# Optimization experiments

Measured on AMD Instinct MI355X. Metric: run time of the kernel, lower is better.

## Reference

```python
import jax, jax.numpy as jnp
import numpy as np

B, N, J, D, H = 64, 128, 512, 1024, 4096
ITERS, EPS = 3, 1e-8
SCALE = D ** -0.5
LN_EPS = 1e-5  # torch LayerNorm default


def _ln(x, g, b):
    m = jnp.mean(x, axis=-1, keepdims=True)
    v = jnp.mean((x - m) ** 2, axis=-1, keepdims=True)
    return (x - m) * jax.lax.rsqrt(v + LN_EPS) * g + b


def setup_inputs() -> dict:
    key = jax.random.key(0)
    ks = jax.random.split(key, 24)
    p = lambda i, shape: jax.random.normal(ks[i], shape, jnp.float32) * 0.02
    return {
        "inputs": jax.random.normal(ks[0], (B, N, D), jnp.float32),
        "texts": jax.random.normal(ks[1], (J, D), jnp.float32),
        "Wq": p(2, (D, D)), "bq": jnp.zeros((D,), jnp.float32),
        "Wk": p(3, (D, D)), "bk": jnp.zeros((D,), jnp.float32),
        "Wv": p(4, (D, D)), "bv": jnp.zeros((D,), jnp.float32),
        "W_ih": p(5, (3 * D, D)), "b_ih": jnp.zeros((3 * D,), jnp.float32),
        "W_hh": p(6, (3 * D, D)), "b_hh": jnp.zeros((3 * D,), jnp.float32),
        "W1": p(7, (H, D)), "b1": jnp.zeros((H,), jnp.float32),
        "W2": p(8, (D, H)), "b2": jnp.zeros((D,), jnp.float32),
        "g_in": jnp.ones((D,), jnp.float32), "be_in": jnp.zeros((D,), jnp.float32),
        "g_sl": jnp.ones((D,), jnp.float32), "be_sl": jnp.zeros((D,), jnp.float32),
        "g_ff": jnp.ones((D,), jnp.float32), "be_ff": jnp.zeros((D,), jnp.float32),
    }


def reference(inputs, texts, Wq, bq, Wk, bk, Wv, bv, W_ih, b_ih, W_hh, b_hh,
              W1, b1, W2, b2, g_in, be_in, g_sl, be_sl, g_ff, be_ff):
    slots = inputs                                  # [B, N, D]
    texts_n = _ln(texts, g_in, be_in)               # [J, D] (repeat == broadcast)
    k = texts_n @ Wk.T + bk                         # [J, D]
    v = texts_n @ Wv.T + bv                         # [J, D]
    for _ in range(ITERS):
        slots_prev = slots
        q = _ln(slots, g_sl, be_sl) @ Wq.T + bq     # [B, N, D]
        dots = jnp.einsum('bid,jd->bij', q, k) * SCALE
        attn = jax.nn.softmax(dots, axis=1) + EPS   # softmax over slots dim
        attn = attn / jnp.sum(attn, axis=-1, keepdims=True)
        updates = jnp.einsum('jd,bij->bid', v, attn)
        # GRUCell: input=updates, hidden=slots_prev (torch gate order r, z, n)
        gi = updates @ W_ih.T + b_ih
        gh = slots_prev @ W_hh.T + b_hh
        i_r, i_z, i_n = jnp.split(gi, 3, axis=-1)
        h_r, h_z, h_n = jnp.split(gh, 3, axis=-1)
        r = jax.nn.sigmoid(i_r + h_r)
        z = jax.nn.sigmoid(i_z + h_z)
        n = jnp.tanh(i_n + r * h_n)
        slots = (1.0 - z) * n + z * slots_prev
        ff = _ln(slots, g_ff, be_ff)
        slots = slots + (jax.nn.relu(ff @ W1.T + b1) @ W2.T + b2)
    return slots
```

## Files before the change

### kernel.cpp

```cpp
#include <hip/hip_runtime.h>
#include <hip/hip_bf16.h>
#include <stdint.h>


using bf16 = __hip_bfloat16;
typedef __bf16 bf16x8 __attribute__((ext_vector_type(8)));
typedef float f32x4 __attribute__((ext_vector_type(4)));

#define F_RELU    1
#define F_SIGMOID 2
#define F_GRU     4
#define F_EPSC    8

__device__ __forceinline__ void gl_to_lds16(const void* g, void* l) {
  __builtin_amdgcn_global_load_lds(
      (const __attribute__((address_space(1))) uint32_t*)(uintptr_t)g,
      (__attribute__((address_space(3))) uint32_t*)(uintptr_t)l,
      16, 0, 0);
}

template <int BN>
__global__ __launch_bounds__(256, 4) void gemm_bt(
    const bf16* __restrict__ X, int ldx,
    const bf16* __restrict__ W, int ldw,
    const float* __restrict__ bias,
    int M, int N, int K, float scale, int flags,
    float* __restrict__ outF, int ldf,
    bf16* __restrict__ outB, int ldb,
    const float* __restrict__ resid,
    const bf16* __restrict__ rz,
    const bf16* __restrict__ hn,
    const float* __restrict__ auxA,
    const float* __restrict__ auxB)
{
  constexpr int NJ = BN / 32;
  __shared__ __align__(16) bf16 As[128 * 64];
  __shared__ __align__(16) bf16 Bs[BN * 64];
  const int t = threadIdx.x;
  const int m0 = blockIdx.x * 128, n0 = blockIdx.y * BN;
  const int wave = t >> 6, lane = t & 63;
  const int wm = (wave >> 1) * 64, wn = (wave & 1) * (BN / 2);
  const int lrow = lane & 15, quad = lane >> 4;

  f32x4 acc[4][NJ] = {};

  const int srow = t >> 3;
  const int scol = ((t & 7) ^ (srow & 7)) * 8;
  const bf16* Ag = X + (size_t)(m0 + srow) * ldx + scol;
  const bf16* Bg = W + (size_t)(n0 + srow) * ldw + scol;
  bf16* Al = As + t * 8;
  bf16* Bl = Bs + t * 8;

  const int r3 = lrow & 7;
  const int c0 = quad ^ r3;
  const int c1 = (4 + quad) ^ r3;

  for (int k0 = 0; k0 < K; k0 += 64) {
#pragma unroll
    for (int u = 0; u < 4; ++u)
      gl_to_lds16(Ag + k0 + (size_t)(u * 32) * ldx, Al + u * 2048);
#pragma unroll
    for (int u = 0; u < NJ; ++u)
      gl_to_lds16(Bg + k0 + (size_t)(u * 32) * ldw, Bl + u * 2048);
    __syncthreads();
    const bf16x8* AS = (const bf16x8*)As;
    const bf16x8* BS = (const bf16x8*)Bs;
#pragma unroll
    for (int kk = 0; kk < 2; ++kk) {
      const int ck = kk ? c1 : c0;
      bf16x8 af[4], bfr[NJ];
#pragma unroll
      for (int i = 0; i < 4; i++)  af[i]  = AS[(wm + i * 16 + lrow) * 8 + ck];
#pragma unroll
      for (int j = 0; j < NJ; j++) bfr[j] = BS[(wn + j * 16 + lrow) * 8 + ck];
#pragma unroll
      for (int i = 0; i < 4; i++)
#pragma unroll
        for (int j = 0; j < NJ; j++)
          acc[i][j] = __builtin_amdgcn_mfma_f32_16x16x32_bf16(af[i], bfr[j], acc[i][j], 0, 0, 0);
    }
    __syncthreads();
  }

#pragma unroll
  for (int i = 0; i < 4; i++) {
    const int row0 = m0 + wm + i * 16 + quad * 4;
#pragma unroll
    for (int j = 0; j < NJ; j++) {
      const int col = n0 + wn + j * 16 + lrow;
      const float badd = bias ? bias[col] : 0.f;
#pragma unroll
      for (int r = 0; r < 4; r++) {
        const int row = row0 + r;
        float val = acc[i][j][r] * scale + badd;
        if (flags & F_EPSC)    val += 1e-8f * auxA[col] * auxB[row];
        if (flags & F_RELU)    val = fmaxf(val, 0.f);
        if (flags & F_SIGMOID) val = 1.f / (1.f + expf(-val));
        if (flags & F_GRU) {
          const size_t ridx = (size_t)row * 1024 + col;
          const float rg = __bfloat162float(rz[(size_t)row * 2048 + col]);
          const float zg = __bfloat162float(rz[(size_t)row * 2048 + 1024 + col]);
          const float hv = __bfloat162float(hn[ridx]);
          const float ng = tanhf(val + rg * hv);
          const float prev = resid[ridx];
          val = (1.f - zg) * ng + zg * prev;
        } else if (resid) {
          val += resid[(size_t)row * ldf + col];
        }
        if (outF) outF[(size_t)row * ldf + col] = val;
        if (outB) outB[(size_t)row * ldb + col] = __float2bfloat16(val);
      }
    }
  }
}

__global__ __launch_bounds__(256) void ln_rows(const float* __restrict__ x,
    const float* __restrict__ g, const float* __restrict__ b,
    bf16* __restrict__ out, int ldo)
{
  const int row = blockIdx.x;
  const int t = threadIdx.x;
  const float* xr = x + (size_t)row * 1024;
  float v[4];
  float s = 0.f, s2 = 0.f;
#pragma unroll
  for (int i = 0; i < 4; i++) {
    float val = xr[t + 256 * i];
    v[i] = val; s += val; s2 += val * val;
  }
#pragma unroll
  for (int off = 32; off > 0; off >>= 1) {
    s  += __shfl_down(s, off);
    s2 += __shfl_down(s2, off);
  }
  __shared__ float rs[4], rs2[4];
  if ((t & 63) == 0) { rs[t >> 6] = s; rs2[t >> 6] = s2; }
  __syncthreads();
  const float S  = rs[0] + rs[1] + rs[2] + rs[3];
  const float S2 = rs2[0] + rs2[1] + rs2[2] + rs2[3];
  const float mean = S * (1.f / 1024.f);
  const float var  = S2 * (1.f / 1024.f) - mean * mean;
  const float rstd = rsqrtf(var + 1e-5f);
  bf16* outr = out + (size_t)row * ldo;
#pragma unroll
  for (int i = 0; i < 4; i++) {
    const int c = t + 256 * i;
    outr[c] = __float2bfloat16((v[i] - mean) * rstd * g[c] + b[c]);
  }
}

__global__ __launch_bounds__(256) void softmax_fused(
    const float* __restrict__ dots, bf16* __restrict__ xcat2,
    float* __restrict__ P)
{
  __shared__ float tile[128][65];
  __shared__ float cred[4][64];
  __shared__ float colmax[64], colinv[64];
  const int b = blockIdx.x, jt = blockIdx.y;
  const int t = threadIdx.x;
  const float* src = dots + (size_t)b * (128 * 512) + jt * 64;
#pragma unroll
  for (int p = 0; p < 32; p++) {
    const int i = p * 4 + (t >> 6), c = t & 63;
    tile[i][c] = src[(size_t)i * 512 + c];
  }
  __syncthreads();
  const int c = t & 63, s = t >> 6;
  float mx = -1e30f;
  for (int i = s * 32; i < s * 32 + 32; i++) mx = fmaxf(mx, tile[i][c]);
  cred[s][c] = mx;
  __syncthreads();
  if (s == 0) colmax[c] = fmaxf(fmaxf(cred[0][c], cred[1][c]),
                                fmaxf(cred[2][c], cred[3][c]));
  __syncthreads();
  const float cm = colmax[c];
  float sum = 0.f;
  for (int i = s * 32; i < s * 32 + 32; i++) {
    const float e = expf(tile[i][c] - cm);
    tile[i][c] = e; sum += e;
  }
  cred[s][c] = sum;
  __syncthreads();
  if (s == 0) colinv[c] = 1.f / (cred[0][c] + cred[1][c] + cred[2][c] + cred[3][c]);
  __syncthreads();
  bf16* dst = xcat2 + (size_t)b * 128 * 1536 + jt * 64;
#pragma unroll
  for (int p = 0; p < 32; p++) {
    const int i = p * 4 + (t >> 6), cc = t & 63;
    dst[(size_t)i * 1536 + cc] = __float2bfloat16(tile[i][cc] * colinv[cc]);
  }
  if (t < 128) {
    float rs = 0.f;
    for (int cc = 0; cc < 64; cc++) rs += tile[t][cc] * colinv[cc];
    P[((size_t)b * 128 + t) * 8 + jt] = rs;
  }
}

__global__ __launch_bounds__(256) void rowinv_k(const float* __restrict__ P,
                                                float* __restrict__ rowinv)
{
  const int m = blockIdx.x * 256 + threadIdx.x;
  const float* p = P + (size_t)m * 8;
  float s = 0.f;
#pragma unroll
  for (int i = 0; i < 8; i++) s += p[i];
  rowinv[m] = 1.f / (s + 512.f * 1e-8f);
}

__global__ __launch_bounds__(256) void smscale(bf16* __restrict__ x,
                                               const float* __restrict__ rinv)
{
  const int idx = blockIdx.x * 256 + threadIdx.x;
  const int m = idx >> 9, j = idx & 511;
  const size_t a = (size_t)m * 1536 + j;
  x[a] = __float2bfloat16(__bfloat162float(x[a]) * rinv[m]);
}

__global__ __launch_bounds__(256) void init_slots(const float* __restrict__ x,
    float* __restrict__ sf, bf16* __restrict__ xr)
{
  const size_t base = (size_t)blockIdx.x * 1024 + threadIdx.x;
#pragma unroll
  for (int i = 0; i < 4; i++) {
    const size_t idx = base + 256 * i;
    const float v = x[idx];
    sf[idx] = v;
    xr[(idx >> 10) * 1536 + (idx & 1023)] = __float2bfloat16(v);
  }
}

__global__ __launch_bounds__(256) void f2b(const float* __restrict__ x,
                                           bf16* __restrict__ y)
{
  const size_t base = (size_t)blockIdx.x * 1024 + threadIdx.x;
#pragma unroll
  for (int i = 0; i < 4; i++) y[base + 256 * i] = __float2bfloat16(x[base + 256 * i]);
}

__global__ __launch_bounds__(256) void f2b_ld(const float* __restrict__ src,
                                              bf16* __restrict__ dst, int dstld)
{
  const int idx = blockIdx.x * 256 + threadIdx.x;
  const int n = idx >> 10, c = idx & 1023;
  dst[(size_t)n * dstld + c] = __float2bfloat16(src[(size_t)n * 1024 + c]);
}

__global__ __launch_bounds__(256) void f2b_T(const float* __restrict__ Wq,
                                             bf16* __restrict__ wqT)
{
  const int idx = blockIdx.x * 256 + threadIdx.x;
  const int d = idx >> 10, dp = idx & 1023;
  wqT[idx] = __float2bfloat16(Wq[(size_t)dp * 1024 + d]);
}

__global__ __launch_bounds__(256) void make_brz(const float* __restrict__ bih,
    const float* __restrict__ bhh, float* __restrict__ brz)
{
  const int n = blockIdx.x * 256 + threadIdx.x;
  brz[n] = bih[n] + bhh[n];
}

__global__ __launch_bounds__(256) void make_bqk(const bf16* __restrict__ k,
    const float* __restrict__ bq, float* __restrict__ bqk, float scale)
{
  const int j = blockIdx.x * 256 + threadIdx.x;
  const bf16* kr = k + (size_t)j * 1024;
  float s = 0.f;
  for (int d = 0; d < 1024; d++) s += bq[d] * __bfloat162float(kr[d]);
  bqk[j] = scale * s;
}

__global__ __launch_bounds__(256) void make_vcol(const bf16* __restrict__ v,
                                                 float* __restrict__ vcol)
{
  const int d = blockIdx.x * 256 + threadIdx.x;
  float s = 0.f;
  for (int j = 0; j < 512; j++) s += __bfloat162float(v[(size_t)j * 1024 + d]);
  vcol[d] = s;
}

__global__ __launch_bounds__(256) void make_c(const float* __restrict__ Wih,
    const float* __restrict__ vcol, float* __restrict__ c)
{
  const int n = blockIdx.x;
  const int t = threadIdx.x;
  const float* wr = Wih + (size_t)n * 1024;
  float s = 0.f;
#pragma unroll
  for (int i = 0; i < 4; i++) s += wr[t + 256 * i] * vcol[t + 256 * i];
#pragma unroll
  for (int off = 32; off > 0; off >>= 1) s += __shfl_down(s, off);
  __shared__ float rs[4];
  if ((t & 63) == 0) rs[t >> 6] = s;
  __syncthreads();
  if (t == 0) c[n] = rs[0] + rs[1] + rs[2] + rs[3];
}

extern "C" void kernel_launch(void* const* d_in, const int* in_sizes, int n_in,
                              void* d_out, int out_size, void* d_ws, size_t ws_size,
                              hipStream_t stream)
{
  const float* inputs = (const float*)d_in[0];
  const float* texts  = (const float*)d_in[1];
  const float* Wq  = (const float*)d_in[2];  const float* bq  = (const float*)d_in[3];
  const float* Wk  = (const float*)d_in[4];  const float* bk  = (const float*)d_in[5];
  const float* Wv  = (const float*)d_in[6];  const float* bv  = (const float*)d_in[7];
  const float* Wih = (const float*)d_in[8];  const float* bih = (const float*)d_in[9];
  const float* Whh = (const float*)d_in[10]; const float* bhh = (const float*)d_in[11];
  const float* W1  = (const float*)d_in[12]; const float* b1  = (const float*)d_in[13];
  const float* W2  = (const float*)d_in[14]; const float* b2  = (const float*)d_in[15];
  const float* g_in = (const float*)d_in[16]; const float* be_in = (const float*)d_in[17];
  const float* g_sl = (const float*)d_in[18]; const float* be_sl = (const float*)d_in[19];
  const float* g_ff = (const float*)d_in[20]; const float* be_ff = (const float*)d_in[21];

  constexpr int B = 64, N = 128, J = 512, D = 1024, H = 4096;
  constexpr int M = B * N;
  const float SCALE = 0.03125f;

  char* ws = (char*)d_ws;
  size_t off = 0;
  auto alloc = [&](size_t bytes) -> char* {
    char* p = ws + off; off += (bytes + 255) & ~(size_t)255; return p;
  };
  bf16* wk_b    = (bf16*)alloc((size_t)D * D * 2);
  bf16* wv_b    = (bf16*)alloc((size_t)D * D * 2);
  bf16* w1_b    = (bf16*)alloc((size_t)H * D * 2);
  bf16* w2_b    = (bf16*)alloc((size_t)D * H * 2);
  bf16* whn_b   = (bf16*)alloc((size_t)D * D * 2);
  bf16* win_b   = (bf16*)alloc((size_t)D * D * 2);
  bf16* wihrz_b = (bf16*)alloc((size_t)2048 * D * 2);
  bf16* wqT_b   = (bf16*)alloc((size_t)D * D * 2);
  bf16* wcat2_b = (bf16*)alloc((size_t)2048 * 1536 * 2);
  bf16* ptn_b   = (bf16*)alloc((size_t)D * J * 2);
  bf16* kq_b    = (bf16*)alloc((size_t)J * D * 2);
  bf16* texts_n = (bf16*)alloc((size_t)J * D * 2);
  bf16* k_b     = (bf16*)alloc((size_t)J * D * 2);
  bf16* v_b     = (bf16*)alloc((size_t)J * D * 2);
  bf16* xcat2_b = (bf16*)alloc((size_t)M * 1536 * 2);
  float* brz_b  = (float*)alloc((size_t)2048 * 4);
  float* bqk_b  = (float*)alloc((size_t)J * 4);
  float* vcol_b = (float*)alloc((size_t)D * 4);
  float* c_b    = (float*)alloc((size_t)3072 * 4);
  float* P_b    = (float*)alloc((size_t)M * 8 * 4);
  float* rinv_b = (float*)alloc((size_t)M * 4);
  char* U = alloc((size_t)48 * 1024 * 1024);
  bf16*  xln_b  = (bf16*)(U);
  float* dots_f = (float*)(U + (size_t)16 * 1024 * 1024);
  bf16*  rz_b   = (bf16*)(U);
  bf16*  hn_b   = (bf16*)(U + (size_t)32 * 1024 * 1024);
  bf16*  h1_b   = (bf16*)(U + (size_t)16 * 1024 * 1024);

  if (ws_size < off) return;

  float* slots_f = (float*)d_out;

  f2b<<<dim3(D * D / 1024), 256, 0, stream>>>(Wk, wk_b);
  f2b<<<dim3(D * D / 1024), 256, 0, stream>>>(Wv, wv_b);
  f2b<<<dim3(H * D / 1024), 256, 0, stream>>>(W1, w1_b);
  f2b<<<dim3(D * H / 1024), 256, 0, stream>>>(W2, w2_b);
  f2b<<<dim3(D * D / 1024), 256, 0, stream>>>(Whh + (size_t)2048 * D, whn_b);
  f2b<<<dim3(D * D / 1024), 256, 0, stream>>>(Wih + (size_t)2048 * D, win_b);
  f2b<<<dim3(2048 * D / 1024), 256, 0, stream>>>(Wih, wihrz_b);
  f2b_T<<<dim3(D * D / 256), 256, 0, stream>>>(Wq, wqT_b);
  f2b_ld<<<dim3(2048 * 1024 / 256), 256, 0, stream>>>(Whh, wcat2_b + 512, 1536);
  make_brz<<<dim3(8), 256, 0, stream>>>(bih, bhh, brz_b);

  init_slots<<<dim3(M * D / 1024), 256, 0, stream>>>(inputs, slots_f, xcat2_b + 512);

  ln_rows<<<dim3(J), 256, 0, stream>>>(texts, g_in, be_in, texts_n, D);
  gemm_bt<64><<<dim3(J / 128, D / 64), 256, 0, stream>>>(
      texts_n, D, wk_b, D, bk, J, D, D, 1.f, 0,
      nullptr, 0, k_b, D, nullptr, nullptr, nullptr, nullptr, nullptr);
  gemm_bt<64><<<dim3(J / 128, D / 64), 256, 0, stream>>>(
      texts_n, D, wv_b, D, bv, J, D, D, 1.f, 0,
      nullptr, 0, v_b, D, nullptr, nullptr, nullptr, nullptr, nullptr);
  gemm_bt<64><<<dim3(J / 128, D / 64), 256, 0, stream>>>(
      k_b, D, wqT_b, D, nullptr, J, D, D, 1.f, 0,
      nullptr, 0, kq_b, D, nullptr, nullptr, nullptr, nullptr, nullptr);
  gemm_bt<64><<<dim3(2048 / 128, J / 64), 256, 0, stream>>>(
      wihrz_b, D, v_b, D, nullptr, 2048, J, D, 1.f, 0,
      nullptr, 0, wcat2_b, 1536, nullptr, nullptr, nullptr, nullptr, nullptr);
  gemm_bt<64><<<dim3(D / 128, J / 64), 256, 0, stream>>>(
      win_b, D, v_b, D, nullptr, D, J, D, 1.f, 0,
      nullptr, 0, ptn_b, J, nullptr, nullptr, nullptr, nullptr, nullptr);
  make_bqk<<<dim3(2), 256, 0, stream>>>(k_b, bq, bqk_b, SCALE);
  make_vcol<<<dim3(4), 256, 0, stream>>>(v_b, vcol_b);
  make_c<<<dim3(3072), 256, 0, stream>>>(Wih, vcol_b, c_b);

  for (int it = 0; it < 3; it++) {
    ln_rows<<<dim3(M), 256, 0, stream>>>(slots_f, g_sl, be_sl, xln_b, D);
    gemm_bt<64><<<dim3(M / 128, J / 64), 256, 0, stream>>>(
        xln_b, D, kq_b, D, bqk_b, M, J, D, SCALE, 0,
        dots_f, J, nullptr, 0, nullptr, nullptr, nullptr, nullptr, nullptr);
    softmax_fused<<<dim3(B, 8), 256, 0, stream>>>(dots_f, xcat2_b, P_b);
    rowinv_k<<<dim3(M / 256), 256, 0, stream>>>(P_b, rinv_b);
    smscale<<<dim3(M * 512 / 256), 256, 0, stream>>>(xcat2_b, rinv_b);
    gemm_bt<64><<<dim3(M / 128, D / 64), 256, 0, stream>>>(
        xcat2_b + 512, 1536, whn_b, D, bhh + 2048, M, D, D, 1.f, 0,
        nullptr, 0, hn_b, D, nullptr, nullptr, nullptr, nullptr, nullptr);
    gemm_bt<128><<<dim3(M / 128, 2048 / 128), 256, 0, stream>>>(
        xcat2_b, 1536, wcat2_b, 1536, brz_b, M, 2048, 1536, 1.f, F_SIGMOID | F_EPSC,
        nullptr, 0, rz_b, 2048, nullptr, nullptr, nullptr, c_b, rinv_b);
    gemm_bt<64><<<dim3(M / 128, D / 64), 256, 0, stream>>>(
        xcat2_b, 1536, ptn_b, J, bih + 2048, M, D, J, 1.f, F_GRU | F_EPSC,
        slots_f, D, xcat2_b + 512, 1536, slots_f, rz_b, hn_b, c_b + 2048, rinv_b);
    ln_rows<<<dim3(M), 256, 0, stream>>>(slots_f, g_ff, be_ff, xln_b, D);
    gemm_bt<128><<<dim3(M / 128, 2048 / 128), 256, 0, stream>>>(
        xln_b, D, w1_b, D, b1, M, 2048, D, 1.f, F_RELU,
        nullptr, 0, h1_b, 2048, nullptr, nullptr, nullptr, nullptr, nullptr);
    gemm_bt<64><<<dim3(M / 128, D / 64), 256, 0, stream>>>(
        h1_b, 2048, w2_b, H, b2, M, D, 2048, 1.f, 0,
        slots_f, D, nullptr, 0, slots_f, nullptr, nullptr, nullptr, nullptr);
    gemm_bt<128><<<dim3(M / 128, 2048 / 128), 256, 0, stream>>>(
        xln_b, D, w1_b + (size_t)2048 * D, D, b1 + 2048, M, 2048, D, 1.f, F_RELU,
        nullptr, 0, h1_b, 2048, nullptr, nullptr, nullptr, nullptr, nullptr);
    gemm_bt<64><<<dim3(M / 128, D / 64), 256, 0, stream>>>(
        h1_b, 2048, w2_b + 2048, H, nullptr, M, D, 2048, 1.f, 0,
        slots_f, D, xcat2_b + 512, 1536, slots_f, nullptr, nullptr, nullptr, nullptr);
  }
}
```

Baseline: 1.611 ms.

## Double-buffer GEMM LDS tiles with async prefetch of next K-slice

The bf16 GEMM kernel now splits K into 32-wide slices held in two LDS buffers, issuing global-to-LDS loads for the next slice before computing on the current one. Manual vmcnt waits and raw barriers replace the __syncthreads pairs so memory latency overlaps the MFMA work. The swizzle is reworked for the narrower tile. The trade-off is twice as many loop iterations, each doing less compute per barrier, and a correctness dependence on hand-tuned waitcnt values.

```diff
diff --git a/kernel.cpp b/kernel.cpp
--- a/kernel.cpp
+++ b/kernel.cpp
@@ -34,8 +34,9 @@
     const float* __restrict__ auxB)
 {
   constexpr int NJ = BN / 32;
-  __shared__ __align__(16) bf16 As[128 * 64];
-  __shared__ __align__(16) bf16 Bs[BN * 64];
+  constexpr int BLOADS = (BN == 128) ? 2 : 1;
+  __shared__ __align__(16) bf16 As[2][128 * 32];
+  __shared__ __align__(16) bf16 Bs[2][BN * 32];
   const int t = threadIdx.x;
   const int m0 = blockIdx.x * 128, n0 = blockIdx.y * BN;
   const int wave = t >> 6, lane = t & 63;
@@ -44,42 +45,53 @@
 
   f32x4 acc[4][NJ] = {};
 
-  const int srow = t >> 3;
-  const int scol = ((t & 7) ^ (srow & 7)) * 8;
+  const int srow = t >> 2;
+  const int scol = ((t & 3) ^ ((t >> 3) & 3)) * 8;
   const bf16* Ag = X + (size_t)(m0 + srow) * ldx + scol;
   const bf16* Bg = W + (size_t)(n0 + srow) * ldw + scol;
-  bf16* Al = As + t * 8;
-  bf16* Bl = Bs + t * 8;
-
-  const int r3 = lrow & 7;
-  const int c0 = quad ^ r3;
-  const int c1 = (4 + quad) ^ r3;
-
-  for (int k0 = 0; k0 < K; k0 += 64) {
-#pragma unroll
-    for (int u = 0; u < 4; ++u)
-      gl_to_lds16(Ag + k0 + (size_t)(u * 32) * ldx, Al + u * 2048);
-#pragma unroll
-    for (int u = 0; u < NJ; ++u)
-      gl_to_lds16(Bg + k0 + (size_t)(u * 32) * ldw, Bl + u * 2048);
-    __syncthreads();
-    const bf16x8* AS = (const bf16x8*)As;
-    const bf16x8* BS = (const bf16x8*)Bs;
-#pragma unroll
-    for (int kk = 0; kk < 2; ++kk) {
-      const int ck = kk ? c1 : c0;
-      bf16x8 af[4], bfr[NJ];
-#pragma unroll
-      for (int i = 0; i < 4; i++)  af[i]  = AS[(wm + i * 16 + lrow) * 8 + ck];
-#pragma unroll
-      for (int j = 0; j < NJ; j++) bfr[j] = BS[(wn + j * 16 + lrow) * 8 + ck];
-#pragma unroll
-      for (int i = 0; i < 4; i++)
-#pragma unroll
-        for (int j = 0; j < NJ; j++)
-          acc[i][j] = __builtin_amdgcn_mfma_f32_16x16x32_bf16(af[i], bfr[j], acc[i][j], 0, 0, 0);
+
+  auto stage = [&](int b, int k0) {
+#pragma unroll
+    for (int u = 0; u < 2; ++u)
+      gl_to_lds16(Ag + k0 + (size_t)(64 * u) * ldx, &As[b][(t + 256 * u) * 8]);
+#pragma unroll
+    for (int u = 0; u < BLOADS; ++u)
+      gl_to_lds16(Bg + k0 + (size_t)(64 * u) * ldw, &Bs[b][(t + 256 * u) * 8]);
+  };
+
+  const int c0 = quad ^ ((lrow >> 1) & 3);
+  const int nt = K >> 5;
+
+  stage(0, 0);
+  for (int tt = 0; tt < nt; ++tt) {
+    const int cur = tt & 1;
+    const bool pf = (tt + 1 < nt);
+    if (pf) stage(cur ^ 1, (tt + 1) << 5);
+    if (pf) {
+      if constexpr (BN == 128) asm volatile("s_waitcnt vmcnt(4)" ::: "memory");
+      else                     asm volatile("s_waitcnt vmcnt(3)" ::: "memory");
+    } else {
+      asm volatile("s_waitcnt vmcnt(0)" ::: "memory");
     }
-    __syncthreads();
+    __builtin_amdgcn_s_barrier();
+    asm volatile("" ::: "memory");
+
+    const bf16x8* AS = (const bf16x8*)As[cur];
+    const bf16x8* BS = (const bf16x8*)Bs[cur];
+    bf16x8 af[4], bfr[NJ];
+#pragma unroll
+    for (int i = 0; i < 4; i++)  af[i]  = AS[(wm + i * 16 + lrow) * 4 + c0];
+#pragma unroll
+    for (int j = 0; j < NJ; j++) bfr[j] = BS[(wn + j * 16 + lrow) * 4 + c0];
+#pragma unroll
+    for (int i = 0; i < 4; i++)
+#pragma unroll
+      for (int j = 0; j < NJ; j++)
+        acc[i][j] = __builtin_amdgcn_mfma_f32_16x16x32_bf16(af[i], bfr[j], acc[i][j], 0, 0, 0);
+
+    asm volatile("s_waitcnt lgkmcnt(0)" ::: "memory");
+    __builtin_amdgcn_s_barrier();
+    asm volatile("" ::: "memory");
   }
 
 #pragma unroll
```

Result: slower. 1.708 ms (+6.0%).

## Fuse hidden-state n-gate GEMM into GRU GEMM with dual accumulators

Applied to the files above, without the earlier changes.

Replaces the separate hn GEMM (slots_prev·W_hn) and the GRU-epilogue GEMM with a single kernel. It runs over the concatenated [attn | slots_bf16] input with a concatenated weight, keeping two accumulator sets: the first 512 K columns feed the input n-gate and the remaining 1024 feed the hidden n-gate. This removes one kernel launch, the bf16 hn round-trip through memory, and one extra read of the A operand. In exchange each block holds twice the accumulator registers, which may reduce occupancy.

```diff
diff --git a/kernel.cpp b/kernel.cpp
--- a/kernel.cpp
+++ b/kernel.cpp
@@ -9,7 +9,6 @@
 
 #define F_RELU    1
 #define F_SIGMOID 2
-#define F_GRU     4
 #define F_EPSC    8
 
 __device__ __forceinline__ void gl_to_lds16(const void* g, void* l) {
@@ -28,8 +27,6 @@
     float* __restrict__ outF, int ldf,
     bf16* __restrict__ outB, int ldb,
     const float* __restrict__ resid,
-    const bf16* __restrict__ rz,
-    const bf16* __restrict__ hn,
     const float* __restrict__ auxA,
     const float* __restrict__ auxB)
 {
@@ -96,19 +93,119 @@
         if (flags & F_EPSC)    val += 1e-8f * auxA[col] * auxB[row];
         if (flags & F_RELU)    val = fmaxf(val, 0.f);
         if (flags & F_SIGMOID) val = 1.f / (1.f + expf(-val));
-        if (flags & F_GRU) {
-          const size_t ridx = (size_t)row * 1024 + col;
-          const float rg = __bfloat162float(rz[(size_t)row * 2048 + col]);
-          const float zg = __bfloat162float(rz[(size_t)row * 2048 + 1024 + col]);
-          const float hv = __bfloat162float(hn[ridx]);
-          const float ng = tanhf(val + rg * hv);
-          const float prev = resid[ridx];
-          val = (1.f - zg) * ng + zg * prev;
-        } else if (resid) {
-          val += resid[(size_t)row * ldf + col];
-        }
+        if (resid) val += resid[(size_t)row * ldf + col];
         if (outF) outF[(size_t)row * ldf + col] = val;
         if (outB) outB[(size_t)row * ldb + col] = __float2bfloat16(val);
+      }
+    }
+  }
+}
+
+__global__ __launch_bounds__(256, 4) void gemm_gru(
+    const bf16* __restrict__ X,
+    const bf16* __restrict__ Wc,
+    const float* __restrict__ bihn,
+    const float* __restrict__ bhhn,
+    const float* __restrict__ cn,
+    const float* __restrict__ rinv,
+    const bf16* __restrict__ rz,
+    float* __restrict__ slots)
+{
+  __shared__ __align__(16) bf16 As[128 * 64];
+  __shared__ __align__(16) bf16 Bs[64 * 64];
+  const int t = threadIdx.x;
+  const int m0 = blockIdx.x * 128, n0 = blockIdx.y * 64;
+  const int wave = t >> 6, lane = t & 63;
+  const int wm = (wave >> 1) * 64, wn = (wave & 1) * 32;
+  const int lrow = lane & 15, quad = lane >> 4;
+
+  f32x4 accN[4][2] = {};
+  f32x4 accH[4][2] = {};
+
+  const int srow = t >> 3;
+  const int scol = ((t & 7) ^ (srow & 7)) * 8;
+  const bf16* Ag = X + (size_t)(m0 + srow) * 1536 + scol;
+  const bf16* Bg = Wc + (size_t)(n0 + srow) * 1536 + scol;
+  bf16* Al = As + t * 8;
+  bf16* Bl = Bs + t * 8;
+
+  const int r3 = lrow & 7;
+  const int c0 = quad ^ r3;
+  const int c1 = (4 + quad) ^ r3;
+
+  for (int k0 = 0; k0 < 512; k0 += 64) {
+#pragma unroll
+    for (int u = 0; u < 4; ++u)
+      gl_to_lds16(Ag + k0 + (size_t)(u * 32) * 1536, Al + u * 2048);
+#pragma unroll
+    for (int u = 0; u < 2; ++u)
+      gl_to_lds16(Bg + k0 + (size_t)(u * 32) * 1536, Bl + u * 2048);
+    __syncthreads();
+    const bf16x8* AS = (const bf16x8*)As;
+    const bf16x8* BS = (const bf16x8*)Bs;
+#pragma unroll
+    for (int kk = 0; kk < 2; ++kk) {
+      const int ck = kk ? c1 : c0;
+      bf16x8 af[4], bfr[2];
+#pragma unroll
+      for (int i = 0; i < 4; i++) af[i] = AS[(wm + i * 16 + lrow) * 8 + ck];
+#pragma unroll
+      for (int j = 0; j < 2; j++) bfr[j] = BS[(wn + j * 16 + lrow) * 8 + ck];
+#pragma unroll
+      for (int i = 0; i < 4; i++)
+#pragma unroll
+        for (int j = 0; j < 2; j++)
+          accN[i][j] = __builtin_amdgcn_mfma_f32_16x16x32_bf16(af[i], bfr[j], accN[i][j], 0, 0, 0);
+    }
+    __syncthreads();
+  }
+  for (int k0 = 512; k0 < 1536; k0 += 64) {
+#pragma unroll
+    for (int u = 0; u < 4; ++u)
+      gl_to_lds16(Ag + k0 + (size_t)(u * 32) * 1536, Al + u * 2048);
+#pragma unroll
+    for (int u = 0; u < 2; ++u)
+      gl_to_lds16(Bg + k0 + (size_t)(u * 32) * 1536, Bl + u * 2048);
+    __syncthreads();
+    const bf16x8* AS = (const bf16x8*)As;
+    const bf16x8* BS = (const bf16x8*)Bs;
+#pragma unroll
+    for (int kk = 0; kk < 2; ++kk) {
+      const int ck = kk ? c1 : c0;
+      bf16x8 af[4], bfr[2];
+#pragma unroll
+      for (int i = 0; i < 4; i++) af[i] = AS[(wm + i * 16 + lrow) * 8 + ck];
+#pragma unroll
+      for (int j = 0; j < 2; j++) bfr[j] = BS[(wn + j * 16 + lrow) * 8 + ck];
+#pragma unroll
+      for (int i = 0; i < 4; i++)
+#pragma unroll
+        for (int j = 0; j < 2; j++)
+          accH[i][j] = __builtin_amdgcn_mfma_f32_16x16x32_bf16(af[i], bfr[j], accH[i][j], 0, 0, 0);
+    }
+    __syncthreads();
+  }
+
+#pragma unroll
+  for (int i = 0; i < 4; i++) {
+    const int row0 = m0 + wm + i * 16 + quad * 4;
+#pragma unroll
+    for (int j = 0; j < 2; j++) {
+      const int col = n0 + wn + j * 16 + lrow;
+      const float bN = bihn[col] + 1e-8f * cn[col] * 0.f;
+      const float bH = bhhn[col];
+      const float cc = cn[col];
+#pragma unroll
+      for (int r = 0; r < 4; r++) {
+        const int row = row0 + r;
+        const size_t ridx = (size_t)row * 1024 + col;
+        const float vn = accN[i][j][r] + bN + 1e-8f * cc * rinv[row];
+        const float vh = accH[i][j][r] + bH;
+        const float rg = __bfloat162float(rz[(size_t)row * 2048 + col]);
+        const float zg = __bfloat162float(rz[(size_t)row * 2048 + 1024 + col]);
+        const float ng = tanhf(vn + rg * vh);
+        const float prev = slots[ridx];
+        slots[ridx] = (1.f - zg) * ng + zg * prev;
       }
     }
   }
@@ -326,12 +423,11 @@
   bf16* wv_b    = (bf16*)alloc((size_t)D * D * 2);
   bf16* w1_b    = (bf16*)alloc((size_t)H * D * 2);
   bf16* w2_b    = (bf16*)alloc((size_t)D * H * 2);
-  bf16* whn_b   = (bf16*)alloc((size_t)D * D * 2);
   bf16* win_b   = (bf16*)alloc((size_t)D * D * 2);
   bf16* wihrz_b = (bf16*)alloc((size_t)2048 * D * 2);
   bf16* wqT_b   = (bf16*)alloc((size_t)D * D * 2);
   bf16* wcat2_b = (bf16*)alloc((size_t)2048 * 1536 * 2);
-  bf16* ptn_b   = (bf16*)alloc((size_t)D * J * 2);
+  bf16* ptnw_b  = (bf16*)alloc((size_t)D * 1536 * 2);
   bf16* kq_b    = (bf16*)alloc((size_t)J * D * 2);
   bf16* texts_n = (bf16*)alloc((size_t)J * D * 2);
   bf16* k_b     = (bf16*)alloc((size_t)J * D * 2);
@@ -346,9 +442,9 @@
   char* U = alloc((size_t)48 * 1024 * 1024);
   bf16*  xln_b  = (bf16*)(U);
   float* dots_f = (float*)(U + (size_t)16 * 1024 * 1024);
-  bf16*  rz_b   = (bf16*)(U);
-  bf16*  hn_b   = (bf16*)(U + (size_t)32 * 1024 * 1024);
+  bf16*  rz_b   = (bf16*)(U + (size_t)32 * 1024 * 1024);
   bf16*  h1_b   = (bf16*)(U + (size_t)16 * 1024 * 1024);
+  rz_b = (bf16*)(U);
 
   if (ws_size < off) return;
 
@@ -358,11 +454,12 @@
   f2b<<<dim3(D * D / 1024), 256, 0, stream>>>(Wv, wv_b);
   f2b<<<dim3(H * D / 1024), 256, 0, stream>>>(W1, w1_b);
   f2b<<<dim3(D * H / 1024), 256, 0, stream>>>(W2, w2_b);
-  f2b<<<dim3(D * D / 1024), 256, 0, stream>>>(Whh + (size_t)2048 * D, whn_b);
   f2b<<<dim3(D * D / 1024), 256, 0, stream>>>(Wih + (size_t)2048 * D, win_b);
   f2b<<<dim3(2048 * D / 1024), 256, 0, stream>>>(Wih, wihrz_b);
   f2b_T<<<dim3(D * D / 256), 256, 0, stream>>>(Wq, wqT_b);
   f2b_ld<<<dim3(2048 * 1024 / 256), 256, 0, stream>>>(Whh, wcat2_b + 512, 1536);
+  f2b_ld<<<dim3(1024 * 1024 / 256), 256, 0, stream>>>(
+      Whh + (size_t)2048 * D, ptnw_b + 512, 1536);
   make_brz<<<dim3(8), 256, 0, stream>>>(bih, bhh, brz_b);
 
   init_slots<<<dim3(M * D / 1024), 256, 0, stream>>>(inputs, slots_f, xcat2_b + 512);
@@ -370,19 +467,19 @@
   ln_rows<<<dim3(J), 256, 0, stream>>>(texts, g_in, be_in, texts_n, D);
   gemm_bt<64><<<dim3(J / 128, D / 64), 256, 0, stream>>>(
       texts_n, D, wk_b, D, bk, J, D, D, 1.f, 0,
-      nullptr, 0, k_b, D, nullptr, nullptr, nullptr, nullptr, nullptr);
+      nullptr, 0, k_b, D, nullptr, nullptr, nullptr);
   gemm_bt<64><<<dim3(J / 128, D / 64), 256, 0, stream>>>(
       texts_n, D, wv_b, D, bv, J, D, D, 1.f, 0,
-      nullptr, 0, v_b, D, nullptr, nullptr, nullptr, nullptr, nullptr);
+      nullptr, 0, v_b, D, nullptr, nullptr, nullptr);
   gemm_bt<64><<<dim3(J / 128, D / 64), 256, 0, stream>>>(
       k_b, D, wqT_b, D, nullptr, J, D, D, 1.f, 0,
-      nullptr, 0, kq_b, D, nullptr, nullptr, nullptr, nullptr, nullptr);
+      nullptr, 0, kq_b, D, nullptr, nullptr, nullptr);
   gemm_bt<64><<<dim3(2048 / 128, J / 64), 256, 0, stream>>>(
       wihrz_b, D, v_b, D, nullptr, 2048, J, D, 1.f, 0,
-      nullptr, 0, wcat2_b, 1536, nullptr, nullptr, nullptr, nullptr, nullptr);
+      nullptr, 0, wcat2_b, 1536, nullptr, nullptr, nullptr);
   gemm_bt<64><<<dim3(D / 128, J / 64), 256, 0, stream>>>(
       win_b, D, v_b, D, nullptr, D, J, D, 1.f, 0,
-      nullptr, 0, ptn_b, J, nullptr, nullptr, nullptr, nullptr, nullptr);
+      nullptr, 0, ptnw_b, 1536, nullptr, nullptr, nullptr);
   make_bqk<<<dim3(2), 256, 0, stream>>>(k_b, bq, bqk_b, SCALE);
   make_vcol<<<dim3(4), 256, 0, stream>>>(v_b, vcol_b);
   make_c<<<dim3(3072), 256, 0, stream>>>(Wih, vcol_b, c_b);
@@ -391,31 +488,28 @@
     ln_rows<<<dim3(M), 256, 0, stream>>>(slots_f, g_sl, be_sl, xln_b, D);
     gemm_bt<64><<<dim3(M / 128, J / 64), 256, 0, stream>>>(
         xln_b, D, kq_b, D, bqk_b, M, J, D, SCALE, 0,
-        dots_f, J, nullptr, 0, nullptr, nullptr, nullptr, nullptr, nullptr);
+        dots_f, J, nullptr, 0, nullptr, nullptr, nullptr);
     softmax_fused<<<dim3(B, 8), 256, 0, stream>>>(dots_f, xcat2_b, P_b);
     rowinv_k<<<dim3(M / 256), 256, 0, stream>>>(P_b, rinv_b);
     smscale<<<dim3(M * 512 / 256), 256, 0, stream>>>(xcat2_b, rinv_b);
-    gemm_bt<64><<<dim3(M / 128, D / 64), 256, 0, stream>>>(
-        xcat2_b + 512, 1536, whn_b, D, bhh + 2048, M, D, D, 1.f, 0,
-        nullptr, 0, hn_b, D, nullptr, nullptr, nullptr, nullptr, nullptr);
     gemm_bt<128><<<dim3(M / 128, 2048 / 128), 256, 0, stream>>>(
         xcat2_b, 1536, wcat2_b, 1536, brz_b, M, 2048, 1536, 1.f, F_SIGMOID | F_EPSC,
-        nullptr, 0, rz_b, 2048, nullptr, nullptr, nullptr, c_b, rinv_b);
-    gemm_bt<64><<<dim3(M / 128, D / 64), 256, 0, stream>>>(
-        xcat2_b, 1536, ptn_b, J, bih + 2048, M, D, J, 1.f, F_GRU | F_EPSC,
-        slots_f, D, xcat2_b + 512, 1536, slots_f, rz_b, hn_b, c_b + 2048, rinv_b);
+        nullptr, 0, rz_b, 2048, nullptr, c_b, rinv_b);
+    gemm_gru<<<dim3(M / 128, D / 64), 256, 0, stream>>>(
+        xcat2_b, ptnw_b, bih + 2048, bhh + 2048, c_b + 2048, rinv_b,
+        rz_b, slots_f);
     ln_rows<<<dim3(M), 256, 0, stream>>>(slots_f, g_ff, be_ff, xln_b, D);
     gemm_bt<128><<<dim3(M / 128, 2048 / 128), 256, 0, stream>>>(
         xln_b, D, w1_b, D, b1, M, 2048, D, 1.f, F_RELU,
-        nullptr, 0, h1_b, 2048, nullptr, nullptr, nullptr, nullptr, nullptr);
+        nullptr, 0, h1_b, 2048, nullptr, nullptr, nullptr);
     gemm_bt<64><<<dim3(M / 128, D / 64), 256, 0, stream>>>(
         h1_b, 2048, w2_b, H, b2, M, D, 2048, 1.f, 0,
-        slots_f, D, nullptr, 0, slots_f, nullptr, nullptr, nullptr, nullptr);
+        slots_f, D, nullptr, 0, slots_f, nullptr, nullptr);
     gemm_bt<128><<<dim3(M / 128, 2048 / 128), 256, 0, stream>>>(
         xln_b, D, w1_b + (size_t)2048 * D, D, b1 + 2048, M, 2048, D, 1.f, F_RELU,
-        nullptr, 0, h1_b, 2048, nullptr, nullptr, nullptr, nullptr, nullptr);
+        nullptr, 0, h1_b, 2048, nullptr, nullptr, nullptr);
     gemm_bt<64><<<dim3(M / 128, D / 64), 256, 0, stream>>>(
         h1_b, 2048, w2_b + 2048, H, nullptr, M, D, 2048, 1.f, 0,
-        slots_f, D, xcat2_b + 512, 1536, slots_f, nullptr, nullptr, nullptr, nullptr);
-  }
-}
+        slots_f, D, xcat2_b + 512, 1536, slots_f, nullptr, nullptr);
+  }
+}
```

After: 1.395 ms. -13.4%, faster.
